# Kernel optimization log

Measured on AMD Instinct MI355X. Metric: run time of the kernel, lower is better.

The kernel has to match this reference:

```python
import jax, jax.numpy as jnp
import numpy as np

PRIOR_HOURS = 48.0
INIT_TIME = 0.0
K = 13  # nr_ref_time_points (time_space)
L = 200  # time steps (axis_2)
D = 64   # features (axis_3)
B = 64

REF_TIME = jnp.asarray(np.linspace(INIT_TIME, PRIOR_HOURS, K).reshape(K, 1, 1), dtype=jnp.float32)


def setup_inputs() -> dict:
    key = jax.random.key(0)
    ks = jax.random.split(key, 9)
    X = jax.random.normal(ks[0], (B, L, D), dtype=jnp.float32)
    T = jax.random.uniform(ks[1], (B, L, D), dtype=jnp.float32) * PRIOR_HOURS
    M = (jax.random.uniform(ks[2], (B, L, D)) > 0.5).astype(jnp.float32)
    DT = jax.random.uniform(ks[3], (B, L, D), dtype=jnp.float32)
    # trainable weights (keras random_normal initializer, stddev=0.05)
    alpha = jax.random.normal(ks[4], (K, 1, 1), dtype=jnp.float32) * 0.05
    w_v = jax.random.normal(ks[5], (K, L, D), dtype=jnp.float32) * 0.05
    w_t = jax.random.normal(ks[6], (K, L, D, 4), dtype=jnp.float32) * 0.05
    b_v = jax.random.normal(ks[7], (K, 1, D), dtype=jnp.float32) * 0.05
    b_t = jax.random.normal(ks[8], (K, L, D, 1), dtype=jnp.float32) * 0.05
    return {"X": X, "T": T, "M": M, "DT": DT, "alpha": alpha,
            "w_v": w_v, "w_t": w_t, "b_v": b_v, "b_t": b_t}


def reference(X, T, M, DT, alpha, w_v, w_t, b_v, b_t):
    # broadcast inputs over the K reference time points: [B,1,L,D] -> [B,K,L,D]
    dist = jnp.abs(T[:, None, :, :] - REF_TIME)                 # [B,K,L,D]
    kernel = jnp.exp(-jax.nn.relu(alpha) * dist)                # [B,K,L,D]
    intensity = jax.nn.relu(X[:, None, :, :] * kernel)          # [B,K,L,D]
    shp = intensity.shape
    x = jnp.broadcast_to(X[:, None, :, :], shp)
    dt = jnp.broadcast_to(DT[:, None, :, :], shp)
    m = jnp.broadcast_to(M[:, None, :, :], shp)
    feat = jnp.stack([x, dt, intensity, m], axis=-1)            # [B,K,L,D,4]
    # stage 1: weighted reduce over the 4-feature axis (b_t broadcasts over it)
    lat = jax.nn.relu(jnp.sum(w_t * feat + b_t, axis=-1))       # [B,K,L,D]
    # stage 2: weighted reduce over the time-step axis L (b_v broadcasts over it)
    out = jax.nn.relu(jnp.sum(w_v * lat + b_v, axis=2))         # [B,K,D]
    return out
```

## Files before the change

### kernel.cpp

```cpp
#include <hip/hip_runtime.h>


#define NB 64
#define NK 13
#define NL 200
#define ND 64

__global__ __launch_bounds__(256) void alnn_kernel(
    const float* __restrict__ X, const float* __restrict__ T,
    const float* __restrict__ M, const float* __restrict__ DT,
    const float* __restrict__ alpha, const float* __restrict__ w_v,
    const float* __restrict__ w_t, const float* __restrict__ b_v,
    const float* __restrict__ b_t, float* __restrict__ out)
{
    const int bk = blockIdx.x;
    const int b = bk / NK;
    const int k = bk % NK;
    const int tid = threadIdx.x;
    const int d  = tid & 63;
    const int lg = tid >> 6;

    const float a    = fmaxf(alpha[k], 0.0f);
    const float reft = 4.0f * (float)k;

    float acc = 0.0f;
    #pragma unroll 2
    for (int l = lg; l < NL; l += 4) {
        const int idx_in = (b * NL + l) * ND + d;
        const int idx_w  = (k * NL + l) * ND + d;
        const float x  = X[idx_in];
        const float t  = T[idx_in];
        const float m  = M[idx_in];
        const float dt = DT[idx_in];
        const float4 wt = ((const float4*)w_t)[idx_w];
        const float bt  = b_t[idx_w];
        const float wv  = w_v[idx_w];

        const float dist  = fabsf(t - reft);
        const float kern  = __expf(-a * dist);
        const float inten = fmaxf(x * kern, 0.0f);
        float s = wt.x * x + wt.y * dt + wt.z * inten + wt.w * m + 4.0f * bt;
        const float lat = fmaxf(s, 0.0f);
        acc = fmaf(wv, lat, acc);
    }

    __shared__ float red[4][64];
    red[lg][d] = acc;
    __syncthreads();
    if (lg == 0) {
        float s = red[0][d] + red[1][d] + red[2][d] + red[3][d];
        s += (float)NL * b_v[k * ND + d];
        out[(b * NK + k) * ND + d] = fmaxf(s, 0.0f);
    }
}

extern "C" void kernel_launch(void* const* d_in, const int* in_sizes, int n_in,
                              void* d_out, int out_size, void* d_ws, size_t ws_size,
                              hipStream_t stream) {
    const float* X     = (const float*)d_in[0];
    const float* T     = (const float*)d_in[1];
    const float* M     = (const float*)d_in[2];
    const float* DT    = (const float*)d_in[3];
    const float* alpha = (const float*)d_in[4];
    const float* w_v   = (const float*)d_in[5];
    const float* w_t   = (const float*)d_in[6];
    const float* b_v   = (const float*)d_in[7];
    const float* b_t   = (const float*)d_in[8];
    float* out = (float*)d_out;

    alnn_kernel<<<NB * NK, 256, 0, stream>>>(X, T, M, DT, alpha, w_v, w_t, b_v, b_t, out);
}
```

Measured before the change: 102.8 us.

## Tile over batch groups and L chunks to reuse weights, reduce via atomics

Restructures the kernel so each block handles one reference time point, eight batches and a chunk of twenty time steps. It loads the w_t, b_t and w_v slice once and reuses it across the batches, with float4-vectorized input loads. Partial sums over L chunks are combined with atomicAdd into a zeroed workspace, and a second kernel applies the bias and ReLU. This cuts repeated weight traffic at the cost of a memset, an extra launch and atomic contention.

```diff
diff --git a/kernel.cpp b/kernel.cpp
--- a/kernel.cpp
+++ b/kernel.cpp
@@ -5,52 +5,97 @@
 #define NK 13
 #define NL 200
 #define ND 64
+#define BG 8
+#define LC 20
+#define NLC (NL / LC)
+#define NBG (NB / BG)
 
-__global__ __launch_bounds__(256) void alnn_kernel(
+__global__ __launch_bounds__(320) void alnn_stage1(
     const float* __restrict__ X, const float* __restrict__ T,
     const float* __restrict__ M, const float* __restrict__ DT,
     const float* __restrict__ alpha, const float* __restrict__ w_v,
-    const float* __restrict__ w_t, const float* __restrict__ b_v,
-    const float* __restrict__ b_t, float* __restrict__ out)
+    const float* __restrict__ w_t, const float* __restrict__ b_t,
+    float* __restrict__ ws)
 {
-    const int bk = blockIdx.x;
-    const int b = bk / NK;
-    const int k = bk % NK;
+    const int k   = blockIdx.x / (NBG * NLC);
+    const int s   = blockIdx.x % (NBG * NLC);
+    const int bg  = s & 7;
+    const int lc  = s >> 3;
     const int tid = threadIdx.x;
-    const int d  = tid & 63;
-    const int lg = tid >> 6;
+    const int dq  = tid & 15;
+    const int lsub = tid >> 4;
+    const int l   = lc * LC + lsub;
+    const int d0  = dq * 4;
 
     const float a    = fmaxf(alpha[k], 0.0f);
     const float reft = 4.0f * (float)k;
 
-    float acc = 0.0f;
-    #pragma unroll 2
-    for (int l = lg; l < NL; l += 4) {
-        const int idx_in = (b * NL + l) * ND + d;
-        const int idx_w  = (k * NL + l) * ND + d;
-        const float x  = X[idx_in];
-        const float t  = T[idx_in];
-        const float m  = M[idx_in];
-        const float dt = DT[idx_in];
-        const float4 wt = ((const float4*)w_t)[idx_w];
-        const float bt  = b_t[idx_w];
-        const float wv  = w_v[idx_w];
+    const int wd = (k * NL + l) * ND + d0;
+    const float4* wt4p = (const float4*)w_t;
+    const float4 wtA = wt4p[wd + 0];
+    const float4 wtB = wt4p[wd + 1];
+    const float4 wtC = wt4p[wd + 2];
+    const float4 wtD = wt4p[wd + 3];
+    const float4 bt4 = ((const float4*)b_t)[wd >> 2];
+    const float4 wv4 = ((const float4*)w_v)[wd >> 2];
 
-        const float dist  = fabsf(t - reft);
-        const float kern  = __expf(-a * dist);
-        const float inten = fmaxf(x * kern, 0.0f);
-        float s = wt.x * x + wt.y * dt + wt.z * inten + wt.w * m + 4.0f * bt;
-        const float lat = fmaxf(s, 0.0f);
-        acc = fmaf(wv, lat, acc);
+    const float4* X4  = (const float4*)X;
+    const float4* T4  = (const float4*)T;
+    const float4* M4  = (const float4*)M;
+    const float4* DT4 = (const float4*)DT;
+
+    float4 acc[BG];
+
+#define COMP(c, wt)  {                                                   \
+        const float dist  = fabsf(t4.c - reft);                          \
+        const float kern  = __expf(-a * dist);                           \
+        const float inten = fmaxf(x4.c * kern, 0.0f);                    \
+        const float sf = wt.x * x4.c + wt.y * dt4.c + wt.z * inten +     \
+                         wt.w * m4.c + 4.0f * bt4.c;                     \
+        acc[b].c = fmaf(wv4.c, fmaxf(sf, 0.0f), acc[b].c);               \
     }
 
-    __shared__ float red[4][64];
-    red[lg][d] = acc;
+    #pragma unroll 2
+    for (int b = 0; b < BG; ++b) {
+        const int bi = bg * BG + b;
+        const int io = ((bi * NL + l) * ND + d0) >> 2;
+        const float4 x4  = X4[io];
+        const float4 t4  = T4[io];
+        const float4 m4  = M4[io];
+        const float4 dt4 = DT4[io];
+        acc[b] = make_float4(0.f, 0.f, 0.f, 0.f);
+        COMP(x, wtA) COMP(y, wtB) COMP(z, wtC) COMP(w, wtD)
+    }
+#undef COMP
+
+    __shared__ float red[LC][BG][ND];
+    #pragma unroll
+    for (int b = 0; b < BG; ++b)
+        *(float4*)&red[lsub][b][d0] = acc[b];
     __syncthreads();
-    if (lg == 0) {
-        float s = red[0][d] + red[1][d] + red[2][d] + red[3][d];
-        s += (float)NL * b_v[k * ND + d];
-        out[(b * NK + k) * ND + d] = fmaxf(s, 0.0f);
+
+    const float* redf = (const float*)red;
+    for (int s2 = tid; s2 < BG * ND; s2 += 320) {
+        float sum = 0.0f;
+        #pragma unroll
+        for (int ls = 0; ls < LC; ++ls)
+            sum += redf[ls * (BG * ND) + s2];
+        const int b = s2 >> 6;
+        const int d = s2 & 63;
+        const int bi = bg * BG + b;
+        atomicAdd(&ws[(bi * NK + k) * ND + d], sum);
+    }
+}
+
+__global__ __launch_bounds__(256) void alnn_stage2(
+    const float* __restrict__ ws, const float* __restrict__ b_v,
+    float* __restrict__ out)
+{
+    const int idx = blockIdx.x * 256 + threadIdx.x;
+    if (idx < NB * NK * ND) {
+        const int d = idx & 63;
+        const int k = (idx >> 6) % NK;
+        out[idx] = fmaxf(ws[idx] + (float)NL * b_v[k * ND + d], 0.0f);
     }
 }
 
@@ -67,6 +112,9 @@
     const float* b_v   = (const float*)d_in[7];
     const float* b_t   = (const float*)d_in[8];
     float* out = (float*)d_out;
+    float* ws  = (float*)d_ws;
 
-    alnn_kernel<<<NB * NK, 256, 0, stream>>>(X, T, M, DT, alpha, w_v, w_t, b_v, b_t, out);
+    hipMemsetAsync(ws, 0, (size_t)NB * NK * ND * sizeof(float), stream);
+    alnn_stage1<<<NK * NBG * NLC, 320, 0, stream>>>(X, T, M, DT, alpha, w_v, w_t, b_t, ws);
+    alnn_stage2<<<(NB * NK * ND + 255) / 256, 256, 0, stream>>>(ws, b_v, out);
 }
```

New measurement: 112.5 us. +9.4%, slower.

## Process two batches per block with float4-vectorized loads to reuse weights

Applied to the files above, without the earlier changes.

Each block now handles one reference time point and two batch elements, so each w_t/b_t/w_v load is reused across both batches. This halves weight traffic, which dominates since the weights are K× larger than the inputs. Each thread also processes four consecutive features using float4 loads for all inputs and weights, and the final shared-memory reduction is widened to 16 partial rows. The cost is half as many blocks (416), which lowers parallelism, plus higher register pressure per thread.

```diff
diff --git a/kernel.cpp b/kernel.cpp
--- a/kernel.cpp
+++ b/kernel.cpp
@@ -6,51 +6,95 @@
 #define NL 200
 #define ND 64
 
-__global__ __launch_bounds__(256) void alnn_kernel(
+__global__ __launch_bounds__(256) void alnn_fused(
     const float* __restrict__ X, const float* __restrict__ T,
     const float* __restrict__ M, const float* __restrict__ DT,
     const float* __restrict__ alpha, const float* __restrict__ w_v,
     const float* __restrict__ w_t, const float* __restrict__ b_v,
     const float* __restrict__ b_t, float* __restrict__ out)
 {
-    const int bk = blockIdx.x;
-    const int b = bk / NK;
-    const int k = bk % NK;
+    const int k   = blockIdx.x >> 5;
+    const int bp  = blockIdx.x & 31;
     const int tid = threadIdx.x;
-    const int d  = tid & 63;
-    const int lg = tid >> 6;
+    const int dq  = tid & 15;
+    const int d0  = dq << 2;
+    const int lsub = tid >> 4;
 
     const float a    = fmaxf(alpha[k], 0.0f);
     const float reft = 4.0f * (float)k;
 
-    float acc = 0.0f;
-    #pragma unroll 2
-    for (int l = lg; l < NL; l += 4) {
-        const int idx_in = (b * NL + l) * ND + d;
-        const int idx_w  = (k * NL + l) * ND + d;
-        const float x  = X[idx_in];
-        const float t  = T[idx_in];
-        const float m  = M[idx_in];
-        const float dt = DT[idx_in];
-        const float4 wt = ((const float4*)w_t)[idx_w];
-        const float bt  = b_t[idx_w];
-        const float wv  = w_v[idx_w];
+    const float4* X4  = (const float4*)X;
+    const float4* T4  = (const float4*)T;
+    const float4* M4  = (const float4*)M;
+    const float4* DT4 = (const float4*)DT;
+    const float4* WT4 = (const float4*)w_t;
+    const float4* BT4 = (const float4*)b_t;
+    const float4* WV4 = (const float4*)w_v;
 
-        const float dist  = fabsf(t - reft);
-        const float kern  = __expf(-a * dist);
-        const float inten = fmaxf(x * kern, 0.0f);
-        float s = wt.x * x + wt.y * dt + wt.z * inten + wt.w * m + 4.0f * bt;
-        const float lat = fmaxf(s, 0.0f);
-        acc = fmaf(wv, lat, acc);
+    const int b0 = bp << 1;
+    const int b1 = b0 + 1;
+
+    float4 acc0 = make_float4(0.f, 0.f, 0.f, 0.f);
+    float4 acc1 = make_float4(0.f, 0.f, 0.f, 0.f);
+
+#define COMP(c, wt, acc) {                                                \
+        const float dist  = fabsf(t4.c - reft);                           \
+        const float kern  = __expf(-a * dist);                            \
+        const float inten = fmaxf(x4.c * kern, 0.0f);                     \
+        const float sf = wt.x * x4.c + wt.y * dt4.c + wt.z * inten +      \
+                         wt.w * m4.c + 4.0f * bt4.c;                      \
+        acc.c = fmaf(wv4.c, fmaxf(sf, 0.0f), acc.c);                      \
     }
 
-    __shared__ float red[4][64];
-    red[lg][d] = acc;
+    #pragma unroll 2
+    for (int j = 0; j < 13; ++j) {
+        const int l = (j << 4) + lsub;
+        if (l < NL) {
+            const int wd = (k * NL + l) * ND + d0;
+            const float4 wtA = WT4[wd + 0];
+            const float4 wtB = WT4[wd + 1];
+            const float4 wtC = WT4[wd + 2];
+            const float4 wtD = WT4[wd + 3];
+            const float4 bt4 = BT4[wd >> 2];
+            const float4 wv4 = WV4[wd >> 2];
+            {
+                const int io = ((b0 * NL + l) * ND + d0) >> 2;
+                const float4 x4  = X4[io];
+                const float4 t4  = T4[io];
+                const float4 m4  = M4[io];
+                const float4 dt4 = DT4[io];
+                COMP(x, wtA, acc0) COMP(y, wtB, acc0)
+                COMP(z, wtC, acc0) COMP(w, wtD, acc0)
+            }
+            {
+                const int io = ((b1 * NL + l) * ND + d0) >> 2;
+                const float4 x4  = X4[io];
+                const float4 t4  = T4[io];
+                const float4 m4  = M4[io];
+                const float4 dt4 = DT4[io];
+                COMP(x, wtA, acc1) COMP(y, wtB, acc1)
+                COMP(z, wtC, acc1) COMP(w, wtD, acc1)
+            }
+        }
+    }
+#undef COMP
+
+    __shared__ float4 red[16][2][16];
+    red[lsub][0][dq] = acc0;
+    red[lsub][1][dq] = acc1;
     __syncthreads();
-    if (lg == 0) {
-        float s = red[0][d] + red[1][d] + red[2][d] + red[3][d];
+
+    if (tid < 128) {
+        const int b = tid >> 6;
+        const int d = tid & 63;
+        const float* redf = (const float*)red;
+        float s = 0.0f;
+        #pragma unroll
+        for (int ls = 0; ls < 16; ++ls)
+            s += redf[ls * 128 + b * 64 + d];
+        const int bi = b0 + b;
         s += (float)NL * b_v[k * ND + d];
-        out[(b * NK + k) * ND + d] = fmaxf(s, 0.0f);
+        out[(bi * NK + k) * ND + d] = fmaxf(s, 0.0f);
     }
 }
 
@@ -68,5 +112,5 @@
     const float* b_t   = (const float*)d_in[8];
     float* out = (float*)d_out;
 
-    alnn_kernel<<<NB * NK, 256, 0, stream>>>(X, T, M, DT, alpha, w_v, w_t, b_v, b_t, out);
+    alnn_fused<<<NK * 32, 256, 0, stream>>>(X, T, M, DT, alpha, w_v, w_t, b_v, b_t, out);
 }
```

New measurement: 94.14 us. -8.4%, faster.
